# Kernel optimization log

Hardware: AMD Instinct MI355X
Metric: run time of the kernel (lower is better)

Reference implementation:

```python
import jax, jax.numpy as jnp
import numpy as np

D = 768      # input_dim
O = 768      # output_dim
E = 8        # num_experts
H = 10 * D   # expert hidden dim (fixed by module: input_dim * 10)
N = 4096     # tokens


def setup_inputs() -> dict:
    key = jax.random.key(0)
    ks = jax.random.split(key, 7)
    s = lambda fan_in: 1.0 / np.sqrt(fan_in)
    x  = jax.random.normal(ks[0], (N, D), dtype=jnp.float32)
    Wg = jax.random.uniform(ks[1], (D, E), jnp.float32, -s(D), s(D))
    bg = jax.random.uniform(ks[2], (E,),   jnp.float32, -s(D), s(D))
    W1 = jax.random.uniform(ks[3], (E, D, H), jnp.float32, -s(D), s(D))
    b1 = jax.random.uniform(ks[4], (E, H),    jnp.float32, -s(D), s(D))
    W2 = jax.random.uniform(ks[5], (E, H, O), jnp.float32, -s(H), s(H))
    b2 = jax.random.uniform(ks[6], (E, O),    jnp.float32, -s(H), s(H))
    return {"x": x, "Wg": Wg, "bg": bg, "W1": W1, "b1": b1, "W2": W2, "b2": b2}


def reference(x, Wg, bg, W1, b1, W2, b2):
    # gating: softmax over experts, keep only top-1 prob (rest zeroed)
    gate_probs = jax.nn.softmax(x @ Wg + bg, axis=1)          # [N, E]
    top_vals, top_idx = jax.lax.top_k(gate_probs, 1)           # [N, 1]
    gate_masked = jnp.zeros_like(gate_probs).at[
        jnp.arange(x.shape[0]), top_idx[:, 0]].set(top_vals[:, 0])
    # dense all-experts MLP (module computes every expert for every token)
    h = jax.nn.relu(jnp.einsum('nd,edh->neh', x, W1) + b1)     # [N, E, H]
    expert_out = jnp.einsum('neh,eho->neo', h, W2) + b2        # [N, E, O]
    # bmm combine: [N,1,E] @ [N,E,O] -> [N,O]
    return jnp.einsum('ne,neo->no', gate_masked, expert_out)
```

## Files before the change

kernel.cpp:

```cpp
#include <hip/hip_runtime.h>
#include <hip/hip_bf16.h>
#include <stdint.h>

#define N_TOK 4096
#define DIM   768
#define NE    8
#define HDIM  7680
#define ODIM  768
#define MAXTILES 40

typedef __bf16 bf16x8 __attribute__((ext_vector_type(8)));
typedef float f32x4 __attribute__((ext_vector_type(4)));

__device__ __forceinline__ unsigned short f2bf(float f) {
    union { float f; unsigned u; } v; v.f = f;
    return (unsigned short)((v.u + 0x7fffu + ((v.u >> 16) & 1u)) >> 16);
}

__device__ __forceinline__ unsigned cvt_pk_bf16(float lo, float hi) {
    unsigned r;
    asm("v_cvt_pk_bf16_f32 %0, %1, %2" : "=v"(r) : "v"(lo), "v"(hi));
    return r;
}

__device__ __forceinline__ void gload_lds16(const unsigned short* g, unsigned short* l) {
    __builtin_amdgcn_global_load_lds(
        (const __attribute__((address_space(1))) unsigned int*)g,
        (__attribute__((address_space(3))) unsigned int*)l, 16, 0, 0);
}

__global__ void moe_gating(const float* __restrict__ x, const float* __restrict__ Wg,
                           const float* __restrict__ bg, int* __restrict__ cnt,
                           int* __restrict__ top_e, int* __restrict__ rnk,
                           float* __restrict__ top_p) {
    const int wid  = threadIdx.x >> 6;
    const int lane = threadIdx.x & 63;
    const int t = blockIdx.x * 4 + wid;
    double p[NE];
#pragma unroll
    for (int j = 0; j < NE; ++j) p[j] = 0.0;
    const float* xr  = x  + (size_t)t * DIM + lane * 12;
    const float* wr0 = Wg + lane * 12 * NE;
#pragma unroll
    for (int i = 0; i < 12; ++i) {
        double xv = (double)xr[i];
#pragma unroll
        for (int j = 0; j < NE; ++j) p[j] += xv * (double)wr0[i * NE + j];
    }
#pragma unroll
    for (int off = 32; off >= 1; off >>= 1)
#pragma unroll
        for (int j = 0; j < NE; ++j) p[j] += __shfl_xor(p[j], off, 64);
    if (lane == 0) {
        double l[NE];
#pragma unroll
        for (int j = 0; j < NE; ++j) l[j] = p[j] + (double)bg[j];
        int be = 0; double bl = l[0];
#pragma unroll
        for (int j = 1; j < NE; ++j) if (l[j] > bl) { bl = l[j]; be = j; }
        double s = 0.0;
#pragma unroll
        for (int j = 0; j < NE; ++j) s += exp(l[j] - bl);
        int rk = atomicAdd(&cnt[be], 1);
        top_e[t] = be; rnk[t] = rk; top_p[t] = (float)(1.0 / s);
    }
}

__global__ void moe_init(int* cnt) { if (threadIdx.x < NE) cnt[threadIdx.x] = 0; }

__global__ void moe_scan(const int* __restrict__ cnt, int* __restrict__ offs,
                         int* __restrict__ tbl, int* __restrict__ ntt) {
    if (threadIdx.x == 0) {
        int s = 0, nt = 0;
        for (int e = 0; e < NE; ++e) {
            offs[e] = s;
            int m = (cnt[e] + 127) >> 7;
            for (int i = 0; i < m; ++i) tbl[nt++] = (e << 8) | i;
            s += cnt[e];
        }
        ntt[0] = nt;
    }
}

__global__ void moe_mkperm(const int* __restrict__ top_e, const int* __restrict__ rnk,
                           const float* __restrict__ top_p, const int* __restrict__ offs,
                           int* __restrict__ perm, float* __restrict__ gate_s) {
    int t = blockIdx.x * 256 + threadIdx.x;
    int e = top_e[t];
    int slot = offs[e] + rnk[t];
    perm[slot] = t;
    gate_s[slot] = top_p[t];
}

__global__ void moe_gather(const float* __restrict__ x, const int* __restrict__ perm,
                           unsigned short* __restrict__ Xg) {
    int slot = blockIdx.x;
    int t = perm[slot];
    const float* src = x + (size_t)t * DIM;
    unsigned short* dst = Xg + (size_t)slot * DIM;
    for (int i = threadIdx.x; i < DIM; i += 256) dst[i] = f2bf(src[i]);
}

__global__ void moe_initout(const int* __restrict__ top_e, const float* __restrict__ top_p,
                            const float* __restrict__ b2, float* __restrict__ out) {
    int t = blockIdx.x;
    int e = top_e[t];
    float gv = top_p[t];
    const float* b = b2 + (size_t)e * ODIM;
    float* o = out + (size_t)t * ODIM;
    for (int i = threadIdx.x; i < ODIM; i += 256) o[i] = gv * b[i];
}

template<int LAYER>
__global__ __launch_bounds__(256, 4) void moe_gemm(
    const unsigned short* __restrict__ A, const float* __restrict__ B,
    const float* __restrict__ bias, const int* __restrict__ cnt,
    const int* __restrict__ offs, const int* __restrict__ perm,
    const float* __restrict__ gate_s, const int* __restrict__ tbl,
    const int* __restrict__ ntt, unsigned short* __restrict__ H,
    float* __restrict__ out) {

    constexpr int NT    = (LAYER == 1) ? HDIM : ODIM;
    constexpr int AST   = (LAYER == 1) ? DIM  : HDIM;
    constexpr int KFULL = (LAYER == 1) ? DIM  : HDIM;
    constexpr int KBLK  = (LAYER == 1) ? DIM  : HDIM / 4;
    constexpr int NITER = KBLK / 32;

    const int ent = blockIdx.y;
    if (ent >= ntt[0]) return;
    const int tt = tbl[ent];
    const int e  = tt >> 8;
    const int mt = tt & 255;
    const int ks = (LAYER == 1) ? 0 : blockIdx.z;
    const int ne = cnt[e];
    const int base = offs[e];
    const int n0 = blockIdx.x * 128;
    const int mlim = ne - mt * 128;
    const int kbase = ks * KBLK;

    __shared__ unsigned short As[2][4096];
    __shared__ unsigned short Bs[2][4096];

    const int tid = threadIdx.x;
    const int lane = tid & 63, w = tid >> 6;
    const int wr = w >> 1, wc = w & 1;
    const int g = lane >> 4, r = lane & 15;

    const int rl0 = 2 * w * 16 + r;
    const int rl1 = rl0 + 16;
    const int cr0 = rl0 < mlim ? rl0 : mlim - 1;
    const int cr1 = rl1 < mlim ? rl1 : mlim - 1;
    const unsigned short* aS0 = A + (size_t)(base + mt * 128 + cr0) * AST + kbase + g * 8;
    const unsigned short* aS1 = A + (size_t)(base + mt * 128 + cr1) * AST + kbase + g * 8;
    const int aD0 = (2 * w) * 512;
    const int aD1 = aD0 + 512;

    const int bn = tid & 127;
    const int kh = tid >> 7;
    const float* bS = B + (size_t)e * KFULL * NT + (size_t)(kbase + kh * 16) * NT + n0 + bn;
    const int bD = (bn >> 4) * 512 + (kh * 2) * 128 + (bn & 15) * 8;

    f32x4 acc[4][4] = {};
    float bv[16];

#define STAGE(t_, buf_)                                                        \
    do {                                                                       \
        int koff_ = (t_) * 32;                                                 \
        gload_lds16(aS0 + koff_, &As[buf_][aD0]);                              \
        gload_lds16(aS1 + koff_, &As[buf_][aD1]);                              \
        const float* bp_ = bS + (size_t)koff_ * NT;                            \
        _Pragma("unroll")                                                      \
        for (int i_ = 0; i_ < 16; ++i_) bv[i_] = bp_[(size_t)i_ * NT];         \
    } while (0)

#define COMMITB(buf_)                                                          \
    do {                                                                       \
        uint4 q0_, q1_;                                                        \
        q0_.x = cvt_pk_bf16(bv[0],  bv[1]);  q0_.y = cvt_pk_bf16(bv[2],  bv[3]);  \
        q0_.z = cvt_pk_bf16(bv[4],  bv[5]);  q0_.w = cvt_pk_bf16(bv[6],  bv[7]);  \
        q1_.x = cvt_pk_bf16(bv[8],  bv[9]);  q1_.y = cvt_pk_bf16(bv[10], bv[11]); \
        q1_.z = cvt_pk_bf16(bv[12], bv[13]); q1_.w = cvt_pk_bf16(bv[14], bv[15]); \
        *(uint4*)&Bs[buf_][bD]       = q0_;                                    \
        *(uint4*)&Bs[buf_][bD + 128] = q1_;                                    \
    } while (0)

    STAGE(0, 0);
    COMMITB(0);
    __syncthreads();

    int cur = 0;
    for (int t = 0; t < NITER; ++t) {
        const bool last = (t == NITER - 1);
        if (!last) STAGE(t + 1, cur ^ 1);
        __builtin_amdgcn_sched_barrier(0);
        bf16x8 af[4], bf[4];
#pragma unroll
        for (int m = 0; m < 4; ++m)
            af[m] = *(const bf16x8*)&As[cur][(wr * 4 + m) * 512 + lane * 8];
#pragma unroll
        for (int n = 0; n < 4; ++n)
            bf[n] = *(const bf16x8*)&Bs[cur][(wc * 4 + n) * 512 + lane * 8];
#pragma unroll
        for (int n = 0; n < 4; ++n)
#pragma unroll
            for (int m = 0; m < 4; ++m)
                acc[m][n] = __builtin_amdgcn_mfma_f32_16x16x32_bf16(af[m], bf[n], acc[m][n], 0, 0, 0);
        if (!last) {
            COMMITB(cur ^ 1);
            __syncthreads();
            cur ^= 1;
        }
    }
#undef STAGE
#undef COMMITB

#pragma unroll
    for (int m = 0; m < 4; ++m) {
#pragma unroll
        for (int j = 0; j < 4; ++j) {
            int lrow = mt * 128 + wr * 64 + m * 16 + g * 4 + j;
            if (lrow < ne) {
                int slot = base + lrow;
#pragma unroll
                for (int n = 0; n < 4; ++n) {
                    int col = n0 + wc * 64 + n * 16 + r;
                    if constexpr (LAYER == 1) {
                        float v = acc[m][n][j] + bias[(size_t)e * NT + col];
                        v = fmaxf(v, 0.0f);
                        H[(size_t)slot * HDIM + col] = f2bf(v);
                    } else {
                        atomicAdd(&out[(size_t)perm[slot] * ODIM + col],
                                  gate_s[slot] * acc[m][n][j]);
                    }
                }
            }
        }
    }
}

extern "C" void kernel_launch(void* const* d_in, const int* in_sizes, int n_in,
                              void* d_out, int out_size, void* d_ws, size_t ws_size,
                              hipStream_t stream) {
    const float* x  = (const float*)d_in[0];
    const float* Wg = (const float*)d_in[1];
    const float* bg = (const float*)d_in[2];
    const float* W1 = (const float*)d_in[3];
    const float* b1 = (const float*)d_in[4];
    const float* W2 = (const float*)d_in[5];
    const float* b2 = (const float*)d_in[6];
    float* out = (float*)d_out;

    char* ws = (char*)d_ws;
    int*   cnt    = (int*)(ws + 0);
    int*   offs   = (int*)(ws + 64);
    int*   ntt    = (int*)(ws + 96);
    int*   tbl    = (int*)(ws + 128);
    int*   top_e  = (int*)(ws + 1024);
    int*   rnk    = (int*)(ws + 1024 + 16384);
    float* top_p  = (float*)(ws + 1024 + 2 * 16384);
    int*   perm   = (int*)(ws + 1024 + 3 * 16384);
    float* gate_s = (float*)(ws + 1024 + 4 * 16384);
    unsigned short* Xg = (unsigned short*)(ws + 82944);
    unsigned short* H  = (unsigned short*)(ws + 82944 + (size_t)N_TOK * DIM * 2);

    moe_init<<<1, 64, 0, stream>>>(cnt);
    moe_gating<<<N_TOK / 4, 256, 0, stream>>>(x, Wg, bg, cnt, top_e, rnk, top_p);
    moe_scan<<<1, 64, 0, stream>>>(cnt, offs, tbl, ntt);
    moe_mkperm<<<N_TOK / 256, 256, 0, stream>>>(top_e, rnk, top_p, offs, perm, gate_s);
    moe_gather<<<N_TOK, 256, 0, stream>>>(x, perm, Xg);
    moe_initout<<<N_TOK, 256, 0, stream>>>(top_e, top_p, b2, out);

    moe_gemm<1><<<dim3(HDIM / 128, MAXTILES, 1), 256, 0, stream>>>(
        Xg, W1, b1, cnt, offs, perm, gate_s, tbl, ntt, H, out);
    moe_gemm<2><<<dim3(ODIM / 128, MAXTILES, 4), 256, 0, stream>>>(
        H, W2, b2, cnt, offs, perm, gate_s, tbl, ntt, H, out);
}
```

Measured before the change: 412.4 us.

## Deepen B-prefetch pipeline to two stages with manual waitcnts and swap grid axes

After: 409.2 us. About the same (-0.8%).

```diff
diff --git a/kernel.cpp b/kernel.cpp
--- a/kernel.cpp
+++ b/kernel.cpp
@@ -112,7 +112,7 @@
 }
 
 template<int LAYER>
-__global__ __launch_bounds__(256, 4) void moe_gemm(
+__global__ __launch_bounds__(256, 3) void moe_gemm(
     const unsigned short* __restrict__ A, const float* __restrict__ B,
     const float* __restrict__ bias, const int* __restrict__ cnt,
     const int* __restrict__ offs, const int* __restrict__ perm,
@@ -126,7 +126,7 @@
     constexpr int KBLK  = (LAYER == 1) ? DIM  : HDIM / 4;
     constexpr int NITER = KBLK / 32;
 
-    const int ent = blockIdx.y;
+    const int ent = blockIdx.x;
     if (ent >= ntt[0]) return;
     const int tt = tbl[ent];
     const int e  = tt >> 8;
@@ -134,7 +134,7 @@
     const int ks = (LAYER == 1) ? 0 : blockIdx.z;
     const int ne = cnt[e];
     const int base = offs[e];
-    const int n0 = blockIdx.x * 128;
+    const int n0 = blockIdx.y * 128;
     const int mlim = ne - mt * 128;
     const int kbase = ks * KBLK;
 
@@ -161,58 +161,87 @@
     const int bD = (bn >> 4) * 512 + (kh * 2) * 128 + (bn & 15) * 8;
 
     f32x4 acc[4][4] = {};
-    float bv[16];
-
-#define STAGE(t_, buf_)                                                        \
-    do {                                                                       \
-        int koff_ = (t_) * 32;                                                 \
-        gload_lds16(aS0 + koff_, &As[buf_][aD0]);                              \
-        gload_lds16(aS1 + koff_, &As[buf_][aD1]);                              \
-        const float* bp_ = bS + (size_t)koff_ * NT;                            \
+    float bvA[16], bvB[16];
+
+#define FENCE __builtin_amdgcn_sched_barrier(0)
+
+#define LOADB(dst_, t_)                                                        \
+    do { const float* bp_ = bS + (size_t)((t_) * 32) * NT;                     \
         _Pragma("unroll")                                                      \
-        for (int i_ = 0; i_ < 16; ++i_) bv[i_] = bp_[(size_t)i_ * NT];         \
+        for (int i_ = 0; i_ < 16; ++i_) dst_[i_] = bp_[(size_t)i_ * NT];       \
     } while (0)
 
-#define COMMITB(buf_)                                                          \
-    do {                                                                       \
-        uint4 q0_, q1_;                                                        \
-        q0_.x = cvt_pk_bf16(bv[0],  bv[1]);  q0_.y = cvt_pk_bf16(bv[2],  bv[3]);  \
-        q0_.z = cvt_pk_bf16(bv[4],  bv[5]);  q0_.w = cvt_pk_bf16(bv[6],  bv[7]);  \
-        q1_.x = cvt_pk_bf16(bv[8],  bv[9]);  q1_.y = cvt_pk_bf16(bv[10], bv[11]); \
-        q1_.z = cvt_pk_bf16(bv[12], bv[13]); q1_.w = cvt_pk_bf16(bv[14], bv[15]); \
+#define DMA_A(t_, buf_)                                                        \
+    do { gload_lds16(aS0 + (t_) * 32, &As[buf_][aD0]);                         \
+         gload_lds16(aS1 + (t_) * 32, &As[buf_][aD1]); } while (0)
+
+#define COMMITB(src_, buf_)                                                    \
+    do { uint4 q0_, q1_;                                                       \
+        q0_.x = cvt_pk_bf16(src_[0],  src_[1]);  q0_.y = cvt_pk_bf16(src_[2],  src_[3]);  \
+        q0_.z = cvt_pk_bf16(src_[4],  src_[5]);  q0_.w = cvt_pk_bf16(src_[6],  src_[7]);  \
+        q1_.x = cvt_pk_bf16(src_[8],  src_[9]);  q1_.y = cvt_pk_bf16(src_[10], src_[11]); \
+        q1_.z = cvt_pk_bf16(src_[12], src_[13]); q1_.w = cvt_pk_bf16(src_[14], src_[15]); \
         *(uint4*)&Bs[buf_][bD]       = q0_;                                    \
         *(uint4*)&Bs[buf_][bD + 128] = q1_;                                    \
     } while (0)
 
-    STAGE(0, 0);
-    COMMITB(0);
-    __syncthreads();
-
-    int cur = 0;
-    for (int t = 0; t < NITER; ++t) {
-        const bool last = (t == NITER - 1);
-        if (!last) STAGE(t + 1, cur ^ 1);
-        __builtin_amdgcn_sched_barrier(0);
-        bf16x8 af[4], bf[4];
-#pragma unroll
-        for (int m = 0; m < 4; ++m)
-            af[m] = *(const bf16x8*)&As[cur][(wr * 4 + m) * 512 + lane * 8];
-#pragma unroll
-        for (int n = 0; n < 4; ++n)
-            bf[n] = *(const bf16x8*)&Bs[cur][(wc * 4 + n) * 512 + lane * 8];
-#pragma unroll
-        for (int n = 0; n < 4; ++n)
-#pragma unroll
-            for (int m = 0; m < 4; ++m)
-                acc[m][n] = __builtin_amdgcn_mfma_f32_16x16x32_bf16(af[m], bf[n], acc[m][n], 0, 0, 0);
-        if (!last) {
-            COMMITB(cur ^ 1);
-            __syncthreads();
-            cur ^= 1;
-        }
-    }
-#undef STAGE
+#define BODY(t_, cur_, LDst_, CMsrc_, MODE_)                                   \
+    do {                                                                       \
+        bf16x8 af_[4], bf_[4];                                                 \
+        _Pragma("unroll")                                                      \
+        for (int m_ = 0; m_ < 4; ++m_)                                         \
+            af_[m_] = *(const bf16x8*)&As[cur_][(wr * 4 + m_) * 512 + lane * 8]; \
+        _Pragma("unroll")                                                      \
+        for (int n_ = 0; n_ < 4; ++n_)                                         \
+            bf_[n_] = *(const bf16x8*)&Bs[cur_][(wc * 4 + n_) * 512 + lane * 8]; \
+        FENCE;                                                                 \
+        if (MODE_ >= 1) DMA_A((t_) + 1, (cur_) ^ 1);                           \
+        FENCE;                                                                 \
+        if (MODE_ == 2) LOADB(LDst_, (t_) + 2);                                \
+        asm volatile("s_waitcnt lgkmcnt(0)" ::: "memory");                     \
+        FENCE;                                                                 \
+        _Pragma("unroll")                                                      \
+        for (int n_ = 0; n_ < 4; ++n_)                                         \
+            _Pragma("unroll")                                                  \
+            for (int m_ = 0; m_ < 4; ++m_)                                     \
+                acc[m_][n_] = __builtin_amdgcn_mfma_f32_16x16x32_bf16(         \
+                    af_[m_], bf_[n_], acc[m_][n_], 0, 0, 0);                   \
+        FENCE;                                                                 \
+        if (MODE_ == 2) { asm volatile("s_waitcnt vmcnt(16)" ::: "memory"); }  \
+        else if (MODE_ == 1) { asm volatile("s_waitcnt vmcnt(0)" ::: "memory"); } \
+        if (MODE_ >= 1) {                                                      \
+            COMMITB(CMsrc_, (cur_) ^ 1);                                       \
+            asm volatile("s_waitcnt lgkmcnt(0)" ::: "memory");                 \
+            __builtin_amdgcn_s_barrier();                                      \
+            FENCE;                                                             \
+        }                                                                      \
+    } while (0)
+
+    LOADB(bvA, 0);
+    FENCE;
+    DMA_A(0, 0);
+    FENCE;
+    LOADB(bvB, 1);
+    asm volatile("s_waitcnt vmcnt(16)" ::: "memory");
+    FENCE;
+    COMMITB(bvA, 0);
+    asm volatile("s_waitcnt lgkmcnt(0)" ::: "memory");
+    __builtin_amdgcn_s_barrier();
+    FENCE;
+
+#pragma unroll 1
+    for (int t = 0; t + 4 <= NITER; t += 2) {
+        BODY(t,     0, bvA, bvB, 2);
+        BODY(t + 1, 1, bvB, bvA, 2);
+    }
+    BODY(NITER - 2, 0, bvA, bvB, 1);
+    BODY(NITER - 1, 1, bvB, bvA, 0);
+
+#undef BODY
 #undef COMMITB
+#undef DMA_A
+#undef LOADB
+#undef FENCE
 
 #pragma unroll
     for (int m = 0; m < 4; ++m) {
@@ -270,8 +299,8 @@
     moe_gather<<<N_TOK, 256, 0, stream>>>(x, perm, Xg);
     moe_initout<<<N_TOK, 256, 0, stream>>>(top_e, top_p, b2, out);
 
-    moe_gemm<1><<<dim3(HDIM / 128, MAXTILES, 1), 256, 0, stream>>>(
+    moe_gemm<1><<<dim3(MAXTILES, HDIM / 128, 1), 256, 0, stream>>>(
         Xg, W1, b1, cnt, offs, perm, gate_s, tbl, ntt, H, out);
-    moe_gemm<2><<<dim3(ODIM / 128, MAXTILES, 4), 256, 0, stream>>>(
+    moe_gemm<2><<<dim3(MAXTILES, ODIM / 128, 4), 256, 0, stream>>>(
         H, W2, b2, cnt, offs, perm, gate_s, tbl, ntt, H, out);
 }
```
